# Kernel optimization log

Measured on AMD Instinct MI355X. Metric: run time of the kernel, lower is better.

The kernel has to match this reference:

```python
import jax, jax.numpy as jnp
import numpy as np

B, T = 4, 96
IN_DIM, OUT_DIM, HID = 16, 16, 16
REL = 2 * IN_DIM  # until=True -> cat(interval max, interval min)
BIG = 1e9


def interval_pooling(a, reduction):
    # a: [b, t, t, d]; out[b,i,j] = reduce over a[b,k,l] for all i<=k<=l<=j
    t = a.shape[1]
    mask = jnp.triu(jnp.ones((t, t), dtype=bool))[None, :, :, None]
    if reduction == 'max':
        fill, cum = -BIG, jax.lax.cummax
    else:
        fill, cum = BIG, jax.lax.cummin
    x = jnp.where(mask, a, fill)
    x = cum(x, axis=1, reverse=True)  # over start k >= i
    x = cum(x, axis=2)                # over end   l <= j
    return jnp.where(mask, x, 0.0)


def dp_step(f, r, W, b):
    # linear_input[b,i,k,j] = cat(f[b,i,k], r[b,k,j]); MLPLogic = Linear+sigmoid;
    # transition_pooling_2d1d = max over k (dim 2). Split W so the wide cubic
    # concat is never materialized (same math as cat + matmul).
    df = f.shape[-1]
    Wf, Wr = W[:df], W[df:]
    ft = jnp.einsum('bikd,dh->bikh', f, Wf)[:, :, :, None, :]  # [b,i,k,1,h]
    rt = jnp.einsum('bkjd,dh->bkjh', r, Wr)[:, None, :, :, :]  # [b,1,k,j,h]
    g = jax.nn.sigmoid(ft + rt + b)  # [b, t+1, t+1, t+1, h] cubic intermediate
    return jnp.max(g, axis=2)        # pool over transition point k


def setup_inputs() -> dict:
    key = jax.random.key(0)
    ks = jax.random.split(key, 7)
    a = jax.random.normal(ks[0], (B, T, T, IN_DIM), jnp.float32)
    W0 = 0.1 * jax.random.normal(ks[1], (REL + REL, HID), jnp.float32)
    b0 = 0.1 * jax.random.normal(ks[2], (HID,), jnp.float32)
    W1 = 0.1 * jax.random.normal(ks[3], (HID + REL + REL, HID), jnp.float32)
    b1 = 0.1 * jax.random.normal(ks[4], (HID,), jnp.float32)
    W2 = 0.1 * jax.random.normal(ks[5], (HID + REL, OUT_DIM), jnp.float32)
    b2 = 0.1 * jax.random.normal(ks[6], (OUT_DIM,), jnp.float32)
    return {'a': a, 'W0': W0, 'b0': b0, 'W1': W1, 'b1': b1, 'W2': W2, 'b2': b2}


def reference(a, W0, b0, W1, b1, W2, b2):
    bsz, t = a.shape[0], a.shape[1]
    r = jnp.concatenate([interval_pooling(a, 'max'),
                         interval_pooling(a, 'min')], axis=-1)  # [b,t,t,2*in]
    f = jnp.zeros((bsz, t + 1, t + 1, r.shape[-1]), a.dtype)
    f = f.at[:, :-1, 1:].set(r)  # pad to boundary indexing [b,t+1,t+1,rel]
    r = f
    # step 0
    f = dp_step(f, r, W0, b0)
    f = jnp.concatenate([f, r], axis=-1)  # residual_input
    # step 1
    f = dp_step(f, r, W1, b1)
    f = jnp.concatenate([f, r], axis=-1)
    # final MLPLogic
    f = jax.nn.sigmoid(f @ W2 + b2)
    return f[:, :-1, 1:]
```

## Files before the change

### kernel.cpp

```cpp
#include <hip/hip_runtime.h>

#define RS   100
#define PLS  9700
#define NP   9409
#define ASTR 34
#define BSTR 68

#define OFF_R   0
#define OFF_A   (OFF_R   + 4*32*PLS)
#define OFF_Bm  (OFF_A   + 4*16*PLS)
#define OFF_F1  (OFF_Bm  + 4*16*PLS)
#define OFF_F2  (OFF_F1  + 4*16*PLS)
#define OFF_A1r (OFF_F2  + 4*16*PLS)
#define OFF_B1  (OFF_A1r + 4*16*PLS)

__device__ __forceinline__ float sigm(float x) { return 1.0f / (1.0f + __expf(-x)); }

__global__ __launch_bounds__(256) void pool_kernel(const float* __restrict__ a, float* __restrict__ R) {
    __shared__ float s[96][97];
    const int tid = threadIdx.x;
    const int b  = blockIdx.x >> 5;
    const int ch = blockIdx.x & 31;
    const int d  = ch & 15;
    const bool isMin = (ch >= 16);

    for (int idx = tid; idx < 96 * 96; idx += 256) {
        int i = idx / 96, j = idx - i * 96;
        float v = a[((size_t)(b * 96 + i) * 96 + j) * 16 + d];
        if (isMin) v = -v;
        s[i][j] = (j >= i) ? v : -1e30f;
    }
    __syncthreads();
    if (tid < 96) {
        int j = tid; float run = -1e30f;
#pragma unroll 4
        for (int i = 95; i >= 0; --i) { run = fmaxf(run, s[i][j]); s[i][j] = run; }
    }
    __syncthreads();
    if (tid < 96) {
        int i = tid; float run = -1e30f;
#pragma unroll 4
        for (int j = 0; j < 96; ++j) { run = fmaxf(run, s[i][j]); s[i][j] = run; }
    }
    __syncthreads();
    float* Rp = R + (size_t)blockIdx.x * PLS;
    for (int idx = tid; idx < 97 * 97; idx += 256) {
        int x = idx / 97, y = idx - x * 97;
        float v = 0.f;
        if (x <= 95 && y >= 1 && x <= y - 1) { v = s[x][y - 1]; if (isMin) v = -v; }
        Rp[x * RS + y] = v;
    }
}

__global__ __launch_bounds__(256) void projA_kernel(const float* __restrict__ R,
                                                    const float* __restrict__ W0, const float* __restrict__ W1,
                                                    float* __restrict__ A0, float* __restrict__ B0,
                                                    float* __restrict__ A1r, float* __restrict__ B1) {
    const int by = blockIdx.y, b = by >> 3, hp = by & 7;
    const int h0 = hp * 2, h1 = h0 + 1;
    const int p = blockIdx.x * 256 + threadIdx.x;
    if (p >= NP) return;
    const int x = p / 97, y = p - x * 97;
    const int off = x * RS + y;
    const float* Rb = R + (size_t)b * 32 * PLS + off;
    float aA00 = 0.f, aA01 = 0.f, aB00 = 0.f, aB01 = 0.f;
    float aA10 = 0.f, aA11 = 0.f, aB10 = 0.f, aB11 = 0.f;
#pragma unroll
    for (int d = 0; d < 32; ++d) {
        const float rv = Rb[(size_t)d * PLS];
        aA00 += rv * W0[d * 16 + h0];
        aA01 += rv * W0[d * 16 + h1];
        aB00 += rv * W0[(32 + d) * 16 + h0];
        aB01 += rv * W0[(32 + d) * 16 + h1];
        aA10 += rv * W1[(16 + d) * 16 + h0];
        aA11 += rv * W1[(16 + d) * 16 + h1];
        aB10 += rv * W1[(48 + d) * 16 + h0];
        aB11 += rv * W1[(48 + d) * 16 + h1];
    }
    const size_t o0 = (size_t)(b * 16 + h0) * PLS + off;
    const size_t o1 = (size_t)(b * 16 + h1) * PLS + off;
    A0 [o0] = aA00;  A0 [o1] = aA01;
    B0 [o0] = aB00;  B0 [o1] = aB01;
    A1r[o0] = aA10;  A1r[o1] = aA11;
    B1 [o0] = aB10;  B1 [o1] = aB11;
}

__global__ __launch_bounds__(256) void projF_kernel(const float* __restrict__ F1, const float* __restrict__ A1r,
                                                    const float* __restrict__ W1, float* __restrict__ A) {
    const int by = blockIdx.y, b = by >> 3, hp = by & 7;
    const int h0 = hp * 2, h1 = h0 + 1;
    const int p = blockIdx.x * 256 + threadIdx.x;
    if (p >= NP) return;
    const int x = p / 97, y = p - x * 97;
    const int off = x * RS + y;
    const float* Fb = F1 + (size_t)b * 16 * PLS + off;
    const size_t o0 = (size_t)(b * 16 + h0) * PLS + off;
    const size_t o1 = (size_t)(b * 16 + h1) * PLS + off;
    float a0 = A1r[o0], a1 = A1r[o1];
#pragma unroll
    for (int c = 0; c < 16; ++c) {
        const float fv = Fb[(size_t)c * PLS];
        a0 += fv * W1[c * 16 + h0];
        a1 += fv * W1[c * 16 + h1];
    }
    A[o0] = a0;
    A[o1] = a1;
}

__global__ __launch_bounds__(256) void maxplus_kernel(const float* __restrict__ A, const float* __restrict__ Bm,
                                                      const float* __restrict__ bias, float* __restrict__ F) {
    __shared__ alignas(16) float As[97 * ASTR];
    __shared__ alignas(16) float Bs[97 * BSTR];
    const int tid = threadIdx.x;
    const int bh = blockIdx.y;
    const int h  = bh & 15;
    const int i0 = (blockIdx.x & 3) * 32;
    const int j0 = (blockIdx.x >> 2) * 64;
    const float* Ab = A  + (size_t)bh * PLS;
    const float* Bb = Bm + (size_t)bh * PLS;

    for (int idx = tid; idx < 32 * 97; idx += 256) {
        int r = idx / 97, k = idx - r * 97;
        int ii = i0 + r;
        As[k * ASTR + r] = (ii <= 96) ? Ab[ii * RS + k] : -1e30f;
    }
    for (int idx = tid; idx < 97 * 16; idx += 256) {
        int k = idx >> 4, q = idx & 15;
        int jj = j0 + q * 4;
        float4 v;
        if (jj + 3 <= 96) {
            v = *reinterpret_cast<const float4*>(&Bb[k * RS + jj]);
        } else {
            v.x = (jj     <= 96) ? Bb[k * RS + jj]     : -1e30f;
            v.y = (jj + 1 <= 96) ? Bb[k * RS + jj + 1] : -1e30f;
            v.z = (jj + 2 <= 96) ? Bb[k * RS + jj + 2] : -1e30f;
            v.w = -1e30f;
        }
        *reinterpret_cast<float4*>(&Bs[k * BSTR + q * 4]) = v;
    }
    __syncthreads();

    const int ty = tid >> 4, tx = tid & 15;
    float acc[2][4];
#pragma unroll
    for (int r = 0; r < 2; ++r)
#pragma unroll
        for (int c = 0; c < 4; ++c) acc[r][c] = -1e30f;

#pragma unroll 4
    for (int k = 0; k < 97; ++k) {
        const float2 a2 = *reinterpret_cast<const float2*>(&As[k * ASTR + ty * 2]);
        const float4 b4 = *reinterpret_cast<const float4*>(&Bs[k * BSTR + tx * 4]);
        acc[0][0] = fmaxf(acc[0][0], a2.x + b4.x);
        acc[0][1] = fmaxf(acc[0][1], a2.x + b4.y);
        acc[0][2] = fmaxf(acc[0][2], a2.x + b4.z);
        acc[0][3] = fmaxf(acc[0][3], a2.x + b4.w);
        acc[1][0] = fmaxf(acc[1][0], a2.y + b4.x);
        acc[1][1] = fmaxf(acc[1][1], a2.y + b4.y);
        acc[1][2] = fmaxf(acc[1][2], a2.y + b4.z);
        acc[1][3] = fmaxf(acc[1][3], a2.y + b4.w);
    }

    const float bb = bias[h];
    float* Fb = F + (size_t)bh * PLS;
    const int row0 = i0 + ty * 2;
    const int col0 = j0 + tx * 4;
#pragma unroll
    for (int r = 0; r < 2; ++r) {
        const int row = row0 + r;
        if (row > 96) continue;
        if (col0 + 3 <= 96) {
            float4 o;
            o.x = sigm(acc[r][0] + bb);
            o.y = sigm(acc[r][1] + bb);
            o.z = sigm(acc[r][2] + bb);
            o.w = sigm(acc[r][3] + bb);
            *reinterpret_cast<float4*>(&Fb[row * RS + col0]) = o;
        } else {
#pragma unroll
            for (int c = 0; c < 4; ++c) {
                const int col = col0 + c;
                if (col <= 96) Fb[row * RS + col] = sigm(acc[r][c] + bb);
            }
        }
    }
}

__global__ __launch_bounds__(256) void final_kernel(const float* __restrict__ R, const float* __restrict__ F2,
                                                    const float* __restrict__ W, const float* __restrict__ bias,
                                                    float* __restrict__ out) {
    const int g = blockIdx.x * 256 + threadIdx.x;
    const int p  = g >> 2;
    const int oq = g & 3;
    const int oj = p % 96;
    const int t1 = p / 96;
    const int i  = t1 % 96;
    const int b  = t1 / 96;
    const int off = i * RS + (oj + 1);
    const float* Fb = F2 + (size_t)b * 16 * PLS + off;
    const float* Rb = R  + (size_t)b * 32 * PLS + off;
    float acc[4];
#pragma unroll
    for (int m = 0; m < 4; ++m) acc[m] = bias[oq * 4 + m];
#pragma unroll
    for (int c = 0; c < 16; ++c) {
        const float fv = Fb[(size_t)c * PLS];
#pragma unroll
        for (int m = 0; m < 4; ++m) acc[m] += fv * W[c * 16 + oq * 4 + m];
    }
#pragma unroll
    for (int d = 0; d < 32; ++d) {
        const float rv = Rb[(size_t)d * PLS];
#pragma unroll
        for (int m = 0; m < 4; ++m) acc[m] += rv * W[(16 + d) * 16 + oq * 4 + m];
    }
    float4 v;
    v.x = sigm(acc[0]);
    v.y = sigm(acc[1]);
    v.z = sigm(acc[2]);
    v.w = sigm(acc[3]);
    *reinterpret_cast<float4*>(out + (size_t)p * 16 + oq * 4) = v;
}

extern "C" void kernel_launch(void* const* d_in, const int* in_sizes, int n_in,
                              void* d_out, int out_size, void* d_ws, size_t ws_size,
                              hipStream_t stream) {
    const float* a  = (const float*)d_in[0];
    const float* W0 = (const float*)d_in[1];
    const float* b0 = (const float*)d_in[2];
    const float* W1 = (const float*)d_in[3];
    const float* b1 = (const float*)d_in[4];
    const float* W2 = (const float*)d_in[5];
    const float* b2 = (const float*)d_in[6];
    float* ws  = (float*)d_ws;
    float* out = (float*)d_out;

    hipLaunchKernelGGL(pool_kernel, dim3(128), dim3(256), 0, stream, a, ws + OFF_R);
    hipLaunchKernelGGL(projA_kernel, dim3(37, 32), dim3(256), 0, stream,
                       ws + OFF_R, W0, W1, ws + OFF_A, ws + OFF_Bm, ws + OFF_A1r, ws + OFF_B1);
    hipLaunchKernelGGL(maxplus_kernel, dim3(8, 64), dim3(256), 0, stream,
                       ws + OFF_A, ws + OFF_Bm, b0, ws + OFF_F1);
    hipLaunchKernelGGL(projF_kernel, dim3(37, 32), dim3(256), 0, stream,
                       ws + OFF_F1, ws + OFF_A1r, W1, ws + OFF_A);
    hipLaunchKernelGGL(maxplus_kernel, dim3(8, 64), dim3(256), 0, stream,
                       ws + OFF_A, ws + OFF_B1, b1, ws + OFF_F2);
    hipLaunchKernelGGL(final_kernel, dim3(576), dim3(256), 0, stream,
                       ws + OFF_R, ws + OFF_F2, W2, b2, out);
}
```

Measured before the change: 152.4 us.

## Fuse max-plus pooling with following projection and final MLP per spatial tile

Replaces the per-channel max-plus kernel plus the separate projF and final kernels with a templated kernel. Each block handles a 16x16 output tile across all 16 hidden channels, so the hidden-dim projection (step-1 input, or the final output MLP) can be applied in shared memory right after the sigmoid. The k dimension is streamed in register-prefetched chunks of 16. This removes two launches and the global round-trips of F1/F2. The trade-offs are a much smaller grid (196 blocks versus 512) and heavier shared-memory use per block.

New measurement: 150.4 us. About the same (-1.3%).

```diff
diff --git a/kernel.cpp b/kernel.cpp
--- a/kernel.cpp
+++ b/kernel.cpp
@@ -3,8 +3,6 @@
 #define RS   100
 #define PLS  9700
 #define NP   9409
-#define ASTR 34
-#define BSTR 68
 
 #define OFF_R   0
 #define OFF_A   (OFF_R   + 4*32*PLS)
@@ -13,6 +11,10 @@
 #define OFF_F2  (OFF_F1  + 4*16*PLS)
 #define OFF_A1r (OFF_F2  + 4*16*PLS)
 #define OFF_B1  (OFF_A1r + 4*16*PLS)
+
+#define HSTR  328
+#define KSTR  20
+#define FSTR  17
 
 __device__ __forceinline__ float sigm(float x) { return 1.0f / (1.0f + __expf(-x)); }
 
@@ -85,141 +87,181 @@
     B1 [o0] = aB10;  B1 [o1] = aB11;
 }
 
-__global__ __launch_bounds__(256) void projF_kernel(const float* __restrict__ F1, const float* __restrict__ A1r,
-                                                    const float* __restrict__ W1, float* __restrict__ A) {
-    const int by = blockIdx.y, b = by >> 3, hp = by & 7;
-    const int h0 = hp * 2, h1 = h0 + 1;
-    const int p = blockIdx.x * 256 + threadIdx.x;
-    if (p >= NP) return;
-    const int x = p / 97, y = p - x * 97;
-    const int off = x * RS + y;
-    const float* Fb = F1 + (size_t)b * 16 * PLS + off;
-    const size_t o0 = (size_t)(b * 16 + h0) * PLS + off;
-    const size_t o1 = (size_t)(b * 16 + h1) * PLS + off;
-    float a0 = A1r[o0], a1 = A1r[o1];
-#pragma unroll
-    for (int c = 0; c < 16; ++c) {
-        const float fv = Fb[(size_t)c * PLS];
-        a0 += fv * W1[c * 16 + h0];
-        a1 += fv * W1[c * 16 + h1];
-    }
-    A[o0] = a0;
-    A[o1] = a1;
-}
-
-__global__ __launch_bounds__(256) void maxplus_kernel(const float* __restrict__ A, const float* __restrict__ Bm,
-                                                      const float* __restrict__ bias, float* __restrict__ F) {
-    __shared__ alignas(16) float As[97 * ASTR];
-    __shared__ alignas(16) float Bs[97 * BSTR];
+template<bool LAST>
+__global__ __launch_bounds__(256) void mp_fused(
+    const float* __restrict__ A, const float* __restrict__ B,
+    const float* __restrict__ biasv,
+    const float* __restrict__ Wx,
+    const float* __restrict__ Aux,
+    const float* __restrict__ bias2,
+    float* __restrict__ Out)
+{
+    __shared__ float As[16 * HSTR];
+    __shared__ float Bs[16 * HSTR];
+    __shared__ float Fs[16 * 16 * FSTR];
+    __shared__ float Ws[768];
+
     const int tid = threadIdx.x;
-    const int bh = blockIdx.y;
-    const int h  = bh & 15;
-    const int i0 = (blockIdx.x & 3) * 32;
-    const int j0 = (blockIdx.x >> 2) * 64;
-    const float* Ab = A  + (size_t)bh * PLS;
-    const float* Bb = Bm + (size_t)bh * PLS;
-
-    for (int idx = tid; idx < 32 * 97; idx += 256) {
-        int r = idx / 97, k = idx - r * 97;
-        int ii = i0 + r;
-        As[k * ASTR + r] = (ii <= 96) ? Ab[ii * RS + k] : -1e30f;
-    }
-    for (int idx = tid; idx < 97 * 16; idx += 256) {
-        int k = idx >> 4, q = idx & 15;
-        int jj = j0 + q * 4;
-        float4 v;
-        if (jj + 3 <= 96) {
-            v = *reinterpret_cast<const float4*>(&Bb[k * RS + jj]);
-        } else {
-            v.x = (jj     <= 96) ? Bb[k * RS + jj]     : -1e30f;
-            v.y = (jj + 1 <= 96) ? Bb[k * RS + jj + 1] : -1e30f;
-            v.z = (jj + 2 <= 96) ? Bb[k * RS + jj + 2] : -1e30f;
-            v.w = -1e30f;
-        }
-        *reinterpret_cast<float4*>(&Bs[k * BSTR + q * 4]) = v;
-    }
-    __syncthreads();
-
-    const int ty = tid >> 4, tx = tid & 15;
-    float acc[2][4];
-#pragma unroll
-    for (int r = 0; r < 2; ++r)
+    const int b  = blockIdx.y;
+    const int ti = blockIdx.x / 7, tj = blockIdx.x % 7;
+    const int i0 = ti * 16, j0 = tj * 16;
+    const int h  = tid >> 4, q = tid & 15;
+    const int iq = q >> 2, jq = q & 3;
+
+    {
+        const int nw = LAST ? 768 : 256;
+        for (int s = tid; s < nw; s += 256) Ws[s] = Wx[s];
+    }
+
+    const float* Ab = A + (size_t)(b * 16 + h) * PLS;
+    const float* Bb = B + (size_t)(b * 16 + h) * PLS;
+
+    float4 Ar[4], Br[4];
+
+    auto load_chunk = [&](int kc) {
+#pragma unroll
+        for (int t = 0; t < 4; ++t) {
+            const int s  = t * 256 + tid;
+            const int h2 = s >> 6;
+            const int m2 = (s >> 2) & 15;
+            const int q2 = s & 3;
+            const float* Ap = A + (size_t)(b * 16 + h2) * PLS;
+            const int row = i0 + m2;
+            if (row <= 96) Ar[t] = *reinterpret_cast<const float4*>(&Ap[row * RS + kc + q2 * 4]);
+            else           Ar[t] = make_float4(-1e30f, -1e30f, -1e30f, -1e30f);
+            const float* Bp = B + (size_t)(b * 16 + h2) * PLS;
+            const int colq = j0 + q2 * 4;
+            if (colq + 3 <= 96) {
+                Br[t] = *reinterpret_cast<const float4*>(&Bp[(kc + m2) * RS + colq]);
+            } else {
+                float v[4];
+#pragma unroll
+                for (int e = 0; e < 4; ++e) {
+                    const int col = colq + e;
+                    v[e] = (col <= 96) ? Bp[(kc + m2) * RS + col] : -1e30f;
+                }
+                Br[t] = make_float4(v[0], v[1], v[2], v[3]);
+            }
+        }
+    };
+    auto store_chunk = [&]() {
+#pragma unroll
+        for (int t = 0; t < 4; ++t) {
+            const int s  = t * 256 + tid;
+            const int h2 = s >> 6;
+            const int m2 = (s >> 2) & 15;
+            const int q2 = s & 3;
+            float* as = &As[h2 * HSTR + m2];
+            as[(q2 * 4 + 0) * KSTR] = Ar[t].x;
+            as[(q2 * 4 + 1) * KSTR] = Ar[t].y;
+            as[(q2 * 4 + 2) * KSTR] = Ar[t].z;
+            as[(q2 * 4 + 3) * KSTR] = Ar[t].w;
+            *reinterpret_cast<float4*>(&Bs[h2 * HSTR + m2 * KSTR + q2 * 4]) = Br[t];
+        }
+    };
+
+    float acc[4][4];
+#pragma unroll
+    for (int r = 0; r < 4; ++r)
 #pragma unroll
         for (int c = 0; c < 4; ++c) acc[r][c] = -1e30f;
 
-#pragma unroll 4
-    for (int k = 0; k < 97; ++k) {
-        const float2 a2 = *reinterpret_cast<const float2*>(&As[k * ASTR + ty * 2]);
-        const float4 b4 = *reinterpret_cast<const float4*>(&Bs[k * BSTR + tx * 4]);
-        acc[0][0] = fmaxf(acc[0][0], a2.x + b4.x);
-        acc[0][1] = fmaxf(acc[0][1], a2.x + b4.y);
-        acc[0][2] = fmaxf(acc[0][2], a2.x + b4.z);
-        acc[0][3] = fmaxf(acc[0][3], a2.x + b4.w);
-        acc[1][0] = fmaxf(acc[1][0], a2.y + b4.x);
-        acc[1][1] = fmaxf(acc[1][1], a2.y + b4.y);
-        acc[1][2] = fmaxf(acc[1][2], a2.y + b4.z);
-        acc[1][3] = fmaxf(acc[1][3], a2.y + b4.w);
-    }
-
-    const float bb = bias[h];
-    float* Fb = F + (size_t)bh * PLS;
-    const int row0 = i0 + ty * 2;
-    const int col0 = j0 + tx * 4;
-#pragma unroll
-    for (int r = 0; r < 2; ++r) {
-        const int row = row0 + r;
-        if (row > 96) continue;
-        if (col0 + 3 <= 96) {
-            float4 o;
-            o.x = sigm(acc[r][0] + bb);
-            o.y = sigm(acc[r][1] + bb);
-            o.z = sigm(acc[r][2] + bb);
-            o.w = sigm(acc[r][3] + bb);
-            *reinterpret_cast<float4*>(&Fb[row * RS + col0]) = o;
-        } else {
-#pragma unroll
-            for (int c = 0; c < 4; ++c) {
-                const int col = col0 + c;
-                if (col <= 96) Fb[row * RS + col] = sigm(acc[r][c] + bb);
-            }
-        }
-    }
-}
-
-__global__ __launch_bounds__(256) void final_kernel(const float* __restrict__ R, const float* __restrict__ F2,
-                                                    const float* __restrict__ W, const float* __restrict__ bias,
-                                                    float* __restrict__ out) {
-    const int g = blockIdx.x * 256 + threadIdx.x;
-    const int p  = g >> 2;
-    const int oq = g & 3;
-    const int oj = p % 96;
-    const int t1 = p / 96;
-    const int i  = t1 % 96;
-    const int b  = t1 / 96;
-    const int off = i * RS + (oj + 1);
-    const float* Fb = F2 + (size_t)b * 16 * PLS + off;
-    const float* Rb = R  + (size_t)b * 32 * PLS + off;
-    float acc[4];
-#pragma unroll
-    for (int m = 0; m < 4; ++m) acc[m] = bias[oq * 4 + m];
-#pragma unroll
-    for (int c = 0; c < 16; ++c) {
-        const float fv = Fb[(size_t)c * PLS];
-#pragma unroll
-        for (int m = 0; m < 4; ++m) acc[m] += fv * W[c * 16 + oq * 4 + m];
-    }
-#pragma unroll
-    for (int d = 0; d < 32; ++d) {
-        const float rv = Rb[(size_t)d * PLS];
-#pragma unroll
-        for (int m = 0; m < 4; ++m) acc[m] += rv * W[(16 + d) * 16 + oq * 4 + m];
-    }
-    float4 v;
-    v.x = sigm(acc[0]);
-    v.y = sigm(acc[1]);
-    v.z = sigm(acc[2]);
-    v.w = sigm(acc[3]);
-    *reinterpret_cast<float4*>(out + (size_t)p * 16 + oq * 4) = v;
+    auto compute_k = [&](int k) {
+        const float4 av = *reinterpret_cast<const float4*>(&As[h * HSTR + k * KSTR + iq * 4]);
+        const float4 bv = *reinterpret_cast<const float4*>(&Bs[h * HSTR + k * KSTR + jq * 4]);
+        const float aa[4] = {av.x, av.y, av.z, av.w};
+        const float bb[4] = {bv.x, bv.y, bv.z, bv.w};
+#pragma unroll
+        for (int r = 0; r < 4; ++r)
+#pragma unroll
+            for (int c = 0; c < 4; ++c) acc[r][c] = fmaxf(acc[r][c], aa[r] + bb[c]);
+    };
+
+    load_chunk(0);
+    store_chunk();
+    __syncthreads();
+    for (int c = 0; c < 6; ++c) {
+        if (c < 5) load_chunk((c + 1) * 16);
+#pragma unroll
+        for (int k = 0; k < 16; ++k) compute_k(k);
+        __syncthreads();
+        if (c < 5) { store_chunk(); __syncthreads(); }
+    }
+    As[h * HSTR + q] = (i0 + q <= 96) ? Ab[(i0 + q) * RS + 96] : -1e30f;
+    Bs[h * HSTR + q] = (j0 + q <= 96) ? Bb[96 * RS + (j0 + q)] : -1e30f;
+    __syncthreads();
+    compute_k(0);
+
+    const float bbia = biasv[h];
+#pragma unroll
+    for (int r = 0; r < 4; ++r)
+#pragma unroll
+        for (int c = 0; c < 4; ++c)
+            Fs[h * (16 * FSTR) + (iq * 4 + r) * FSTR + (jq * 4 + c)] = sigm(acc[r][c] + bbia);
+    __syncthreads();
+
+    if (!LAST) {
+        const float* Axr = Aux + (size_t)(b * 16 + h) * PLS;
+        float* Ob = Out + (size_t)(b * 16 + h) * PLS;
+        const int ybase = j0 + jq * 4;
+        const bool fullq = (ybase + 3 <= 96);
+#pragma unroll
+        for (int r = 0; r < 4; ++r) {
+            const int x = i0 + iq * 4 + r;
+            if (x > 96) continue;
+            float o4[4];
+            if (fullq) {
+                const float4 t4 = *reinterpret_cast<const float4*>(&Axr[x * RS + ybase]);
+                o4[0] = t4.x; o4[1] = t4.y; o4[2] = t4.z; o4[3] = t4.w;
+            } else {
+#pragma unroll
+                for (int e = 0; e < 4; ++e) o4[e] = (ybase + e <= 96) ? Axr[x * RS + ybase + e] : 0.f;
+            }
+#pragma unroll
+            for (int c16 = 0; c16 < 16; ++c16) {
+                const float w = Ws[c16 * 16 + h];
+                const float* fr = &Fs[c16 * (16 * FSTR) + (iq * 4 + r) * FSTR + jq * 4];
+                o4[0] += fr[0] * w; o4[1] += fr[1] * w; o4[2] += fr[2] * w; o4[3] += fr[3] * w;
+            }
+            if (fullq) {
+                *reinterpret_cast<float4*>(&Ob[x * RS + ybase]) = make_float4(o4[0], o4[1], o4[2], o4[3]);
+            } else {
+#pragma unroll
+                for (int e = 0; e < 4; ++e) if (ybase + e <= 96) Ob[x * RS + ybase + e] = o4[e];
+            }
+        }
+    } else {
+        const int pi = tid >> 4, pj = tid & 15;
+        const int x = i0 + pi, y = j0 + pj;
+        if (x <= 95 && y >= 1 && y <= 96) {
+            const float* Rb = Aux + (size_t)b * 32 * PLS + x * RS + y;
+            float o[16];
+#pragma unroll
+            for (int oo = 0; oo < 16; ++oo) o[oo] = bias2[oo];
+#pragma unroll
+            for (int c = 0; c < 16; ++c) {
+                const float fv = Fs[c * (16 * FSTR) + pi * FSTR + pj];
+#pragma unroll
+                for (int oo = 0; oo < 16; ++oo) o[oo] += fv * Ws[c * 16 + oo];
+            }
+#pragma unroll
+            for (int d = 0; d < 32; ++d) {
+                const float rv = Rb[(size_t)d * PLS];
+#pragma unroll
+                for (int oo = 0; oo < 16; ++oo) o[oo] += rv * Ws[(16 + d) * 16 + oo];
+            }
+            float* dst = Out + ((size_t)((b * 96 + x) * 96) + (y - 1)) * 16;
+#pragma unroll
+            for (int qd = 0; qd < 4; ++qd) {
+                float4 v;
+                v.x = sigm(o[qd * 4 + 0]);
+                v.y = sigm(o[qd * 4 + 1]);
+                v.z = sigm(o[qd * 4 + 2]);
+                v.w = sigm(o[qd * 4 + 3]);
+                *reinterpret_cast<float4*>(&dst[qd * 4]) = v;
+            }
+        }
+    }
 }
 
 extern "C" void kernel_launch(void* const* d_in, const int* in_sizes, int n_in,
@@ -238,12 +280,8 @@
     hipLaunchKernelGGL(pool_kernel, dim3(128), dim3(256), 0, stream, a, ws + OFF_R);
     hipLaunchKernelGGL(projA_kernel, dim3(37, 32), dim3(256), 0, stream,
                        ws + OFF_R, W0, W1, ws + OFF_A, ws + OFF_Bm, ws + OFF_A1r, ws + OFF_B1);
-    hipLaunchKernelGGL(maxplus_kernel, dim3(8, 64), dim3(256), 0, stream,
-                       ws + OFF_A, ws + OFF_Bm, b0, ws + OFF_F1);
-    hipLaunchKernelGGL(projF_kernel, dim3(37, 32), dim3(256), 0, stream,
-                       ws + OFF_F1, ws + OFF_A1r, W1, ws + OFF_A);
-    hipLaunchKernelGGL(maxplus_kernel, dim3(8, 64), dim3(256), 0, stream,
-                       ws + OFF_A, ws + OFF_B1, b1, ws + OFF_F2);
-    hipLaunchKernelGGL(final_kernel, dim3(576), dim3(256), 0, stream,
-                       ws + OFF_R, ws + OFF_F2, W2, b2, out);
-}
+    hipLaunchKernelGGL((mp_fused<false>), dim3(49, 4), dim3(256), 0, stream,
+                       ws + OFF_A, ws + OFF_Bm, b0, W1, ws + OFF_A1r, b0, ws + OFF_F1);
+    hipLaunchKernelGGL((mp_fused<true>), dim3(49, 4), dim3(256), 0, stream,
+                       ws + OFF_F1, ws + OFF_B1, b1, W2, ws + OFF_R, b2, out);
+}
```
